# Kernel optimization log

Measured on AMD Instinct MI355X. Metric: run time of the kernel, lower is better.

The kernel has to match this reference:

```python
import jax, jax.numpy as jnp
import numpy as np

N_NODES = 10000
N_EDGES = 160000
NEG_SLOPE = 0.2  # PyG GATConv default leaky_relu slope


def gat_conv(x, src, dst, W, a_src, a_dst, b, heads, out_ch, concat, n):
    # linear projection per head: [n, heads, out_ch]
    h = (x @ W).reshape(n, heads, out_ch)
    # per-node attention logits
    al_s = jnp.sum(h * a_src, axis=-1)  # [n, heads]
    al_d = jnp.sum(h * a_dst, axis=-1)  # [n, heads]
    # per-edge score, softmax over incoming edges of each destination node
    e = jax.nn.leaky_relu(al_s[src] + al_d[dst], NEG_SLOPE)  # [E, heads]
    m = jax.ops.segment_max(e, dst, num_segments=n)
    p = jnp.exp(e - m[dst])
    s = jax.ops.segment_sum(p, dst, num_segments=n)
    alpha = p / (s[dst] + 1e-16)  # [E, heads]
    # weighted scatter-aggregate of source messages
    out = jax.ops.segment_sum(h[src] * alpha[..., None], dst, num_segments=n)
    out = out.reshape(n, heads * out_ch) if concat else out.mean(axis=1)
    return out + b


def setup_inputs() -> dict:
    key = jax.random.key(0)
    ks = jax.random.split(key, 16)
    x = jax.random.normal(ks[0], (N_NODES, 32), dtype=jnp.float32)
    edge_index = jax.random.randint(ks[1], (2, N_EDGES), 0, N_NODES, dtype=jnp.int64)

    def glorot(k, shape):
        fan = shape[0] + shape[-1]
        return jax.random.uniform(k, shape, jnp.float32, -1.0, 1.0) * jnp.sqrt(6.0 / fan)

    # layer 1: 32 -> 8 per head, 8 heads, concat -> 64
    W1 = glorot(ks[2], (32, 64))
    asrc1 = glorot(ks[3], (8, 8))
    adst1 = glorot(ks[4], (8, 8))
    b1 = jnp.zeros((64,), jnp.float32)
    # layer 2: 64 -> 64 per head, 8 heads, concat -> 512
    W2 = glorot(ks[5], (64, 512))
    asrc2 = glorot(ks[6], (8, 64))
    adst2 = glorot(ks[7], (8, 64))
    b2 = jnp.zeros((512,), jnp.float32)
    # layer 3: 512 -> 6, 1 head, no concat
    W3 = glorot(ks[8], (512, 6))
    asrc3 = glorot(ks[9], (1, 6))
    adst3 = glorot(ks[10], (1, 6))
    b3 = jnp.zeros((6,), jnp.float32)

    return dict(x=x, edge_index=edge_index,
                W1=W1, asrc1=asrc1, adst1=adst1, b1=b1,
                W2=W2, asrc2=asrc2, adst2=adst2, b2=b2,
                W3=W3, asrc3=asrc3, adst3=adst3, b3=b3)


def reference(x, edge_index, W1, asrc1, adst1, b1, W2, asrc2, adst2, b2, W3, asrc3, adst3, b3):
    n = x.shape[0]
    # PyG GATConv adds self-loops by default
    loops = jnp.arange(n, dtype=edge_index.dtype)
    src = jnp.concatenate([edge_index[0], loops])
    dst = jnp.concatenate([edge_index[1], loops])
    # dropout layers are identity in eval mode
    h = jax.nn.elu(gat_conv(x, src, dst, W1, asrc1, adst1, b1, 8, 8, True, n))
    h = jax.nn.elu(gat_conv(h, src, dst, W2, asrc2, adst2, b2, 8, 64, True, n))
    out = gat_conv(h, src, dst, W3, asrc3, adst3, b3, 1, 6, False, n)
    return out
```

## Files before the change

kernel.cpp:

```cpp
#include <hip/hip_runtime.h>
#include <hip/hip_bf16.h>
#include <math.h>


#define NEG_SLOPE 0.2f

__device__ __forceinline__ float lrelu(float v) {
  return v > 0.f ? v : NEG_SLOPE * v;
}


__global__ __launch_bounds__(256) void count_deg(const int* __restrict__ ei,
                                                 int* __restrict__ deg, int E) {
  int e = blockIdx.x * blockDim.x + threadIdx.x;
  if (e < E) atomicAdd(&deg[ei[E + e]], 1);
}

__global__ __launch_bounds__(1024) void scan3(const int* __restrict__ deg,
                                              int* __restrict__ rowptr,
                                              int* __restrict__ cursor, int n,
                                              const float* __restrict__ W1,
                                              const float* __restrict__ as1,
                                              const float* __restrict__ ad1,
                                              const float* __restrict__ W2,
                                              const float* __restrict__ as2,
                                              const float* __restrict__ ad2,
                                              float* __restrict__ av) {
  int t = threadIdx.x;
  if (blockIdx.x == 0) {
    __shared__ int part[1024];
    int chunk = (n + 1023) >> 10;
    int lo = t * chunk;
    int hi = min(lo + chunk, n);
    int s = 0;
    for (int i = lo; i < hi; ++i) s += deg[i];
    part[t] = s;
    __syncthreads();
    for (int off = 1; off < 1024; off <<= 1) {
      int v = (t >= off) ? part[t - off] : 0;
      __syncthreads();
      part[t] += v;
      __syncthreads();
    }
    int run = (t == 0) ? 0 : part[t - 1];
    for (int i = lo; i < hi; ++i) {
      rowptr[i] = run;
      cursor[i] = run;
      run += deg[i];
    }
    if (t == 1023) rowptr[n] = part[1023];
  } else if (blockIdx.x == 1) {
    if (t < 256) {
      int h = t >> 5, k = t & 31;
      float s = 0.f, d = 0.f;
#pragma unroll
      for (int c = 0; c < 8; ++c) {
        float w = W1[k * 64 + h * 8 + c];
        s += w * as1[h * 8 + c];
        d += w * ad1[h * 8 + c];
      }
      av[t] = s;
      av[256 + t] = d;
    }
  } else {
    if (t < 512) {
      int h = t >> 6, k = t & 63;
      float s = 0.f, d = 0.f;
#pragma unroll
      for (int c = 0; c < 64; ++c) {
        float w = W2[k * 512 + h * 64 + c];
        s += w * as2[h * 64 + c];
        d += w * ad2[h * 64 + c];
      }
      av[512 + t] = s;
      av[1024 + t] = d;
    }
  }
}

__global__ __launch_bounds__(256) void fill_edges(const int* __restrict__ ei,
                                                  int* __restrict__ cursor,
                                                  int* __restrict__ esrc, int E) {
  int e = blockIdx.x * blockDim.x + threadIdx.x;
  if (e < E) {
    int d = ei[E + e];
    int pos = atomicAdd(&cursor[d], 1);
    esrc[pos] = ei[e];
  }
}


template <int HH, int K>
__global__ __launch_bounds__(256) void logits_x(const float* __restrict__ X,
                                                const float* __restrict__ avs,
                                                const float* __restrict__ avd,
                                                float* __restrict__ als,
                                                float* __restrict__ ald,
                                                float* __restrict__ selfe, int n) {
  int idx = blockIdx.x * blockDim.x + threadIdx.x;
  if (idx >= n * HH) return;
  int node = idx / HH;
  int h = idx - node * HH;
  const float* xr = X + (size_t)node * K;
  const float* vs = avs + h * K;
  const float* vd = avd + h * K;
  float s0 = 0.f, s1 = 0.f;
#pragma unroll
  for (int k4 = 0; k4 < K / 4; ++k4) {
    float4 xv = *reinterpret_cast<const float4*>(&xr[k4 * 4]);
    float4 a = *reinterpret_cast<const float4*>(&vs[k4 * 4]);
    float4 b = *reinterpret_cast<const float4*>(&vd[k4 * 4]);
    s0 += xv.x * a.x + xv.y * a.y + xv.z * a.z + xv.w * a.w;
    s1 += xv.x * b.x + xv.y * b.y + xv.z * b.z + xv.w * b.w;
  }
  als[idx] = s0;
  ald[idx] = s1;
  float e = s0 + s1;
  selfe[idx] = lrelu(e);
}


__global__ __launch_bounds__(256) void msum_alpha8(const int* __restrict__ esrc,
                                                   const float* __restrict__ als,
                                                   const float* __restrict__ ald,
                                                   const float* __restrict__ selfe,
                                                   const int* __restrict__ rowptr,
                                                   float* __restrict__ alpha,
                                                   float* __restrict__ asel, int n) {
  int node = blockIdx.x * 4 + (threadIdx.x >> 6);
  int lane = threadIdx.x & 63;
  if (node >= n) return;
  int i = lane >> 3;
  int h = lane & 7;
  float aldv = ald[node * 8 + h];
  float e0 = selfe[node * 8 + h];
  int r0 = rowptr[node], r1 = rowptr[node + 1];

  float m = e0;
  for (int p = r0 + i; p < r1; p += 8)
    m = fmaxf(m, lrelu(als[esrc[p] * 8 + h] + aldv));
  m = fmaxf(m, __shfl_xor(m, 8, 64));
  m = fmaxf(m, __shfl_xor(m, 16, 64));
  m = fmaxf(m, __shfl_xor(m, 32, 64));

  float s = 0.f;
  for (int p = r0 + i; p < r1; p += 8)
    s += __expf(lrelu(als[esrc[p] * 8 + h] + aldv) - m);
  s += __shfl_xor(s, 8, 64);
  s += __shfl_xor(s, 16, 64);
  s += __shfl_xor(s, 32, 64);
  float a0 = __expf(e0 - m);
  float rs = 1.f / (s + a0 + 1e-16f);
  if (lane < 8) asel[node * 8 + lane] = a0 * rs;

  for (int p = r0 + i; p < r1; p += 8)
    alpha[(size_t)p * 8 + h] = __expf(lrelu(als[esrc[p] * 8 + h] + aldv) - m) * rs;
}

__global__ __launch_bounds__(256) void msum_alpha1(const int* __restrict__ esrc,
                                                   const float* __restrict__ als,
                                                   const float* __restrict__ ald,
                                                   const float* __restrict__ selfe,
                                                   const int* __restrict__ rowptr,
                                                   float* __restrict__ alpha,
                                                   float* __restrict__ asel, int n) {
  int node = blockIdx.x * 4 + (threadIdx.x >> 6);
  int lane = threadIdx.x & 63;
  if (node >= n) return;
  float aldv = ald[node];
  float e0 = selfe[node];
  int r0 = rowptr[node], r1 = rowptr[node + 1];

  float m = e0;
  for (int p = r0 + lane; p < r1; p += 64)
    m = fmaxf(m, lrelu(als[esrc[p]] + aldv));
#pragma unroll
  for (int off = 1; off < 64; off <<= 1) m = fmaxf(m, __shfl_xor(m, off, 64));

  float s = 0.f;
  for (int p = r0 + lane; p < r1; p += 64)
    s += __expf(lrelu(als[esrc[p]] + aldv) - m);
#pragma unroll
  for (int off = 1; off < 64; off <<= 1) s += __shfl_xor(s, off, 64);
  float a0 = __expf(e0 - m);
  float rs = 1.f / (s + a0 + 1e-16f);
  if (lane == 0) asel[node] = a0 * rs;

  for (int p = r0 + lane; p < r1; p += 64)
    alpha[p] = __expf(lrelu(als[esrc[p]] + aldv) - m) * rs;
}


__global__ __launch_bounds__(256) void agg1(const float* __restrict__ X,
                                            const float* __restrict__ alpha,
                                            const float* __restrict__ asel,
                                            const int* __restrict__ rowptr,
                                            const int* __restrict__ esrc,
                                            float* __restrict__ AGG, int n) {
  int node = blockIdx.x * 4 + (threadIdx.x >> 6);
  int lane = threadIdx.x & 63;
  if (node >= n) return;
  int ch = lane & 31;
  int eslot = lane >> 5;
  float acc[8];
  if (eslot == 0) {
    float xs = X[((unsigned)node << 5) + ch];
#pragma unroll
    for (int h = 0; h < 8; ++h) acc[h] = asel[node * 8 + h] * xs;
  } else {
#pragma unroll
    for (int h = 0; h < 8; ++h) acc[h] = 0.f;
  }
  int r0 = rowptr[node], r1 = rowptr[node + 1];
  int p = r0 + eslot;
  for (; p + 2 < r1; p += 4) {
    int s0 = esrc[p], s1 = esrc[p + 2];
    float xv0 = X[((unsigned)s0 << 5) + ch];
    float xv1 = X[((unsigned)s1 << 5) + ch];
    float4 a00 = *reinterpret_cast<const float4*>(&alpha[(size_t)p * 8]);
    float4 a01 = *reinterpret_cast<const float4*>(&alpha[(size_t)p * 8 + 4]);
    float4 a10 = *reinterpret_cast<const float4*>(&alpha[(size_t)(p + 2) * 8]);
    float4 a11 = *reinterpret_cast<const float4*>(&alpha[(size_t)(p + 2) * 8 + 4]);
    acc[0] += a00.x * xv0; acc[1] += a00.y * xv0;
    acc[2] += a00.z * xv0; acc[3] += a00.w * xv0;
    acc[4] += a01.x * xv0; acc[5] += a01.y * xv0;
    acc[6] += a01.z * xv0; acc[7] += a01.w * xv0;
    acc[0] += a10.x * xv1; acc[1] += a10.y * xv1;
    acc[2] += a10.z * xv1; acc[3] += a10.w * xv1;
    acc[4] += a11.x * xv1; acc[5] += a11.y * xv1;
    acc[6] += a11.z * xv1; acc[7] += a11.w * xv1;
  }
  if (p < r1) {
    int s0 = esrc[p];
    float xv0 = X[((unsigned)s0 << 5) + ch];
    float4 a00 = *reinterpret_cast<const float4*>(&alpha[(size_t)p * 8]);
    float4 a01 = *reinterpret_cast<const float4*>(&alpha[(size_t)p * 8 + 4]);
    acc[0] += a00.x * xv0; acc[1] += a00.y * xv0;
    acc[2] += a00.z * xv0; acc[3] += a00.w * xv0;
    acc[4] += a01.x * xv0; acc[5] += a01.y * xv0;
    acc[6] += a01.z * xv0; acc[7] += a01.w * xv0;
  }
#pragma unroll
  for (int h = 0; h < 8; ++h) acc[h] += __shfl_xor(acc[h], 32, 64);
  if (eslot == 0) {
    unsigned base = (unsigned)node * 256 + ch;
#pragma unroll
    for (int h = 0; h < 8; ++h) AGG[base + h * 32] = acc[h];
  }
}

__global__ __launch_bounds__(256) void agg2(const float* __restrict__ X,
                                            const float* __restrict__ alpha,
                                            const float* __restrict__ asel,
                                            const int* __restrict__ rowptr,
                                            const int* __restrict__ esrc,
                                            float* __restrict__ AGG, int n) {
  int node = blockIdx.x * 4 + (threadIdx.x >> 6);
  int lane = threadIdx.x & 63;
  if (node >= n) return;
  float acc[8];
  float xs = X[((unsigned)node << 6) + lane];
#pragma unroll
  for (int h = 0; h < 8; ++h) acc[h] = asel[node * 8 + h] * xs;
  int r0 = rowptr[node], r1 = rowptr[node + 1];
  int p = r0;
  for (; p + 4 <= r1; p += 4) {
    int s0 = esrc[p], s1 = esrc[p + 1], s2 = esrc[p + 2], s3 = esrc[p + 3];
    float xv0 = X[((unsigned)s0 << 6) + lane];
    float xv1 = X[((unsigned)s1 << 6) + lane];
    float xv2 = X[((unsigned)s2 << 6) + lane];
    float xv3 = X[((unsigned)s3 << 6) + lane];
#pragma unroll
    for (int q = 0; q < 4; ++q) {
      float xv = q == 0 ? xv0 : q == 1 ? xv1 : q == 2 ? xv2 : xv3;
      float4 a0 = *reinterpret_cast<const float4*>(&alpha[(size_t)(p + q) * 8]);
      float4 a1 = *reinterpret_cast<const float4*>(&alpha[(size_t)(p + q) * 8 + 4]);
      acc[0] += a0.x * xv; acc[1] += a0.y * xv;
      acc[2] += a0.z * xv; acc[3] += a0.w * xv;
      acc[4] += a1.x * xv; acc[5] += a1.y * xv;
      acc[6] += a1.z * xv; acc[7] += a1.w * xv;
    }
  }
  for (; p < r1; ++p) {
    int s0 = esrc[p];
    float xv = X[((unsigned)s0 << 6) + lane];
    float4 a0 = *reinterpret_cast<const float4*>(&alpha[(size_t)p * 8]);
    float4 a1 = *reinterpret_cast<const float4*>(&alpha[(size_t)p * 8 + 4]);
    acc[0] += a0.x * xv; acc[1] += a0.y * xv;
    acc[2] += a0.z * xv; acc[3] += a0.w * xv;
    acc[4] += a1.x * xv; acc[5] += a1.y * xv;
    acc[6] += a1.z * xv; acc[7] += a1.w * xv;
  }
  unsigned base = (unsigned)node * 512 + lane;
#pragma unroll
  for (int h = 0; h < 8; ++h) AGG[base + h * 64] = acc[h];
}


__global__ __launch_bounds__(256) void proj1(const float* __restrict__ AGG,
                                             const float* __restrict__ W1,
                                             const float* __restrict__ b1,
                                             float* __restrict__ OUT, int n) {
  int w = blockIdx.x * 4 + (threadIdx.x >> 6);
  int lane = threadIdx.x & 63;
  int node0 = w * 8;
  if (node0 >= n) return;
  int h = lane >> 3;
  float acc[8];
#pragma unroll
  for (int j = 0; j < 8; ++j) acc[j] = 0.f;
  for (int k = 0; k < 32; ++k) {
    float wv = W1[k * 64 + lane];
#pragma unroll
    for (int j = 0; j < 8; ++j) {
      int nd = min(node0 + j, n - 1);
      acc[j] += AGG[(unsigned)nd * 256 + h * 32 + k] * wv;
    }
  }
  float bv = b1[lane];
#pragma unroll
  for (int j = 0; j < 8; ++j) {
    int nd = node0 + j;
    if (nd >= n) break;
    float v = acc[j] + bv;
    v = v > 0.f ? v : expm1f(v);
    OUT[(unsigned)nd * 64 + lane] = v;
  }
}

__global__ __launch_bounds__(256) void proj2(const float* __restrict__ AGG,
                                             const float* __restrict__ W2,
                                             const float* __restrict__ b2,
                                             float* __restrict__ OUT, int n) {
  int w = blockIdx.x * 4 + (threadIdx.x >> 6);
  int lane = threadIdx.x & 63;
  int node0 = w * 4;
  if (node0 >= n) return;
  int c0 = lane * 8;
  int h = lane >> 3;
  float acc[4][8];
#pragma unroll
  for (int j = 0; j < 4; ++j)
#pragma unroll
    for (int c = 0; c < 8; ++c) acc[j][c] = 0.f;
  for (int k = 0; k < 64; ++k) {
    const float4 w0 = *reinterpret_cast<const float4*>(&W2[(size_t)k * 512 + c0]);
    const float4 w1 = *reinterpret_cast<const float4*>(&W2[(size_t)k * 512 + c0 + 4]);
#pragma unroll
    for (int j = 0; j < 4; ++j) {
      int nd = min(node0 + j, n - 1);
      float xv = AGG[(unsigned)nd * 512 + h * 64 + k];
      acc[j][0] += xv * w0.x; acc[j][1] += xv * w0.y;
      acc[j][2] += xv * w0.z; acc[j][3] += xv * w0.w;
      acc[j][4] += xv * w1.x; acc[j][5] += xv * w1.y;
      acc[j][6] += xv * w1.z; acc[j][7] += xv * w1.w;
    }
  }
  float4 bv0 = *reinterpret_cast<const float4*>(&b2[c0]);
  float4 bv1 = *reinterpret_cast<const float4*>(&b2[c0 + 4]);
#pragma unroll
  for (int j = 0; j < 4; ++j) {
    int nd = node0 + j;
    if (nd >= n) break;
    float v[8];
    v[0] = acc[j][0] + bv0.x; v[1] = acc[j][1] + bv0.y;
    v[2] = acc[j][2] + bv0.z; v[3] = acc[j][3] + bv0.w;
    v[4] = acc[j][4] + bv1.x; v[5] = acc[j][5] + bv1.y;
    v[6] = acc[j][6] + bv1.z; v[7] = acc[j][7] + bv1.w;
#pragma unroll
    for (int c = 0; c < 8; ++c) v[c] = v[c] > 0.f ? v[c] : expm1f(v[c]);
    float4* o = reinterpret_cast<float4*>(&OUT[(unsigned)nd * 512 + c0]);
    o[0] = make_float4(v[0], v[1], v[2], v[3]);
    o[1] = make_float4(v[4], v[5], v[6], v[7]);
  }
}

__global__ __launch_bounds__(256) void gemm_l3f(const float* __restrict__ X,
                                                const float* __restrict__ W,
                                                const float* __restrict__ As,
                                                const float* __restrict__ Ad,
                                                float* __restrict__ H,
                                                float* __restrict__ als,
                                                float* __restrict__ ald,
                                                float* __restrict__ selfe, int n) {
  int node = blockIdx.x * 4 + (threadIdx.x >> 6);
  int lane = threadIdx.x & 63;
  if (node >= n) return;
  float acc[6] = {0.f, 0.f, 0.f, 0.f, 0.f, 0.f};
  for (int k = lane; k < 512; k += 64) {
    float xv = X[(size_t)node * 512 + k];
#pragma unroll
    for (int c = 0; c < 6; ++c) acc[c] += xv * W[k * 6 + c];
  }
#pragma unroll
  for (int c = 0; c < 6; ++c) {
#pragma unroll
    for (int off = 32; off >= 1; off >>= 1)
      acc[c] += __shfl_down(acc[c], off, 64);
  }
  if (lane == 0) {
    float s0 = 0.f, s1 = 0.f;
#pragma unroll
    for (int c = 0; c < 6; ++c) {
      H[(size_t)node * 6 + c] = acc[c];
      s0 += acc[c] * As[c];
      s1 += acc[c] * Ad[c];
    }
    als[node] = s0;
    ald[node] = s1;
    selfe[node] = lrelu(s0 + s1);
  }
}

__global__ __launch_bounds__(256) void agg_l3(const float* __restrict__ HF,
                                              const float* __restrict__ alpha,
                                              const float* __restrict__ asel,
                                              const float* __restrict__ bias,
                                              const int* __restrict__ rowptr,
                                              const int* __restrict__ esrc,
                                              float* __restrict__ OUT, int n) {
  int node = blockIdx.x * 4 + (threadIdx.x >> 6);
  int lane = threadIdx.x & 63;
  if (node >= n) return;
  int ch = lane < 6 ? lane : 0;
  float acc = asel[node] * HF[(unsigned)node * 6u + ch];
  int r0 = rowptr[node], r1 = rowptr[node + 1];
  int p = r0;
  for (; p + 2 <= r1; p += 2) {
    int s0 = esrc[p], s1 = esrc[p + 1];
    float h0 = HF[(unsigned)s0 * 6u + ch];
    float h1 = HF[(unsigned)s1 * 6u + ch];
    acc += alpha[p] * h0 + alpha[p + 1] * h1;
  }
  if (p < r1) acc += alpha[p] * HF[(unsigned)esrc[p] * 6u + ch];
  if (lane < 6) OUT[(unsigned)node * 6u + lane] = acc + bias[lane];
}


extern "C" void kernel_launch(void* const* d_in, const int* in_sizes, int n_in,
                              void* d_out, int out_size, void* d_ws, size_t ws_size,
                              hipStream_t stream) {
  const float* x     = (const float*)d_in[0];
  const int*   ei    = (const int*)d_in[1];
  const float* W1    = (const float*)d_in[2];
  const float* asrc1 = (const float*)d_in[3];
  const float* adst1 = (const float*)d_in[4];
  const float* b1    = (const float*)d_in[5];
  const float* W2    = (const float*)d_in[6];
  const float* asrc2 = (const float*)d_in[7];
  const float* adst2 = (const float*)d_in[8];
  const float* b2    = (const float*)d_in[9];
  const float* W3    = (const float*)d_in[10];
  const float* asrc3 = (const float*)d_in[11];
  const float* adst3 = (const float*)d_in[12];
  const float* b3    = (const float*)d_in[13];
  float* outf = (float*)d_out;

  const int n = in_sizes[0] / 32;
  const int E = in_sizes[1] / 2;

  char* ws = (char*)d_ws;
  size_t off = 0;
  auto alloc = [&](size_t bytes) {
    size_t o = off;
    off = (off + bytes + 255) & ~(size_t)255;
    return ws + o;
  };
  int* deg     = (int*)alloc((size_t)n * 4);
  int* rowptr  = (int*)alloc((size_t)(n + 1) * 4);
  int* cursor  = (int*)alloc((size_t)n * 4);
  int* esrc    = (int*)alloc((size_t)E * 4);
  float* alpha = (float*)alloc((size_t)E * 8 * 4);
  float* selfe = (float*)alloc((size_t)n * 8 * 4);
  float* als   = (float*)alloc((size_t)n * 8 * 4);
  float* ald   = (float*)alloc((size_t)n * 8 * 4);
  float* asel  = (float*)alloc((size_t)n * 8 * 4);
  float* av    = (float*)alloc((size_t)1536 * 4);
  float* AGG1  = (float*)alloc((size_t)n * 256 * 4);
  float* x1    = (float*)alloc((size_t)n * 64 * 4);
  float* AGG2  = (float*)alloc((size_t)n * 512 * 4);
  float* x2    = (float*)alloc((size_t)n * 512 * 4);
  float* h3    = (float*)alloc((size_t)n * 6 * 4);

  int nb4 = (n + 3) / 4;

  hipMemsetAsync(deg, 0, (size_t)n * 4, stream);
  count_deg<<<(E + 255) / 256, 256, 0, stream>>>(ei, deg, E);
  scan3<<<3, 1024, 0, stream>>>(deg, rowptr, cursor, n,
                                W1, asrc1, adst1, W2, asrc2, adst2, av);
  fill_edges<<<(E + 255) / 256, 256, 0, stream>>>(ei, cursor, esrc, E);

  logits_x<8, 32><<<(n * 8 + 255) / 256, 256, 0, stream>>>(x, av, av + 256, als, ald, selfe, n);
  msum_alpha8<<<nb4, 256, 0, stream>>>(esrc, als, ald, selfe, rowptr, alpha, asel, n);
  agg1<<<nb4, 256, 0, stream>>>(x, alpha, asel, rowptr, esrc, AGG1, n);
  proj1<<<(n / 8 + 3) / 4 + 1, 256, 0, stream>>>(AGG1, W1, b1, x1, n);

  logits_x<8, 64><<<(n * 8 + 255) / 256, 256, 0, stream>>>(x1, av + 512, av + 1024, als, ald, selfe, n);
  msum_alpha8<<<nb4, 256, 0, stream>>>(esrc, als, ald, selfe, rowptr, alpha, asel, n);
  agg2<<<nb4, 256, 0, stream>>>(x1, alpha, asel, rowptr, esrc, AGG2, n);
  proj2<<<(n / 4 + 3) / 4 + 1, 256, 0, stream>>>(AGG2, W2, b2, x2, n);

  gemm_l3f<<<nb4, 256, 0, stream>>>(x2, W3, asrc3, adst3, h3, als, ald, selfe, n);
  msum_alpha1<<<nb4, 256, 0, stream>>>(esrc, als, ald, selfe, rowptr, alpha, asel, n);
  agg_l3<<<nb4, 256, 0, stream>>>(h3, alpha, asel, b3, rowptr, esrc, outf, n);
}
```

Measured before the change: 256.4 us.

## Fuse whole GAT pipeline into one cooperative persistent kernel with grid syncs

Replaces the chain of about fifteen kernel launches with a single cooperative kernel that uses grid.sync between phases. Within each layer it fuses the softmax, the aggregation and the projection, keeping per-node attention weights and aggregates in shared memory so the alpha and AGG intermediates no longer pass through global memory. The goal is to remove launch overhead and that global traffic. In exchange, occupancy is bounded by the cooperative grid size, each grid-wide barrier has a cost, and nodes with more than 96 incoming edges fall back to recomputing exponentials for the overflow edges.

New measurement: 782.0 us. 3.05x slower.

```diff
diff --git a/kernel.cpp b/kernel.cpp
--- a/kernel.cpp
+++ b/kernel.cpp
@@ -1,12 +1,401 @@
 #include <hip/hip_runtime.h>
 #include <hip/hip_bf16.h>
+#include <hip/hip_cooperative_groups.h>
 #include <math.h>
 
 
 #define NEG_SLOPE 0.2f
+#define DCAP 96
+
+namespace cg = cooperative_groups;
 
 __device__ __forceinline__ float lrelu(float v) {
   return v > 0.f ? v : NEG_SLOPE * v;
+}
+
+
+struct CoopP {
+  const float* x; const int* ei;
+  const float* W1; const float* as1; const float* ad1; const float* b1;
+  const float* W2; const float* as2; const float* ad2; const float* b2;
+  const float* W3; const float* as3; const float* ad3; const float* b3;
+  float* outf;
+  int n, E;
+  int* deg; int* rowptr; int* cursor; int* esrc;
+  float* als; float* ald; float* selfe; float* av;
+  float* x1; float* x2; float* h3;
+};
+
+template <int K>
+__device__ __forceinline__ void logits_one(const float* __restrict__ X,
+                                           const float* __restrict__ avs,
+                                           const float* __restrict__ avd,
+                                           float* __restrict__ als,
+                                           float* __restrict__ ald,
+                                           float* __restrict__ selfe, int idx) {
+  int node = idx >> 3;
+  int h = idx & 7;
+  const float* xr = X + (size_t)node * K;
+  const float* vs = avs + h * K;
+  const float* vd = avd + h * K;
+  float s0 = 0.f, s1 = 0.f;
+#pragma unroll
+  for (int k4 = 0; k4 < K / 4; ++k4) {
+    float4 xv = *reinterpret_cast<const float4*>(&xr[k4 * 4]);
+    float4 a = *reinterpret_cast<const float4*>(&vs[k4 * 4]);
+    float4 b = *reinterpret_cast<const float4*>(&vd[k4 * 4]);
+    s0 += xv.x * a.x + xv.y * a.y + xv.z * a.z + xv.w * a.w;
+    s1 += xv.x * b.x + xv.y * b.y + xv.z * b.z + xv.w * b.w;
+  }
+  als[idx] = s0;
+  ald[idx] = s1;
+  selfe[idx] = lrelu(s0 + s1);
+}
+
+__global__ __launch_bounds__(256, 4) void gat_coop(CoopP P) {
+  cg::grid_group grid = cg::this_grid();
+  const int t = threadIdx.x;
+  const int lane = t & 63;
+  const int w = t >> 6;
+  const int bid = blockIdx.x;
+  const int nb = gridDim.x;
+  const int tid = bid * 256 + t;
+  const int nthr = nb * 256;
+  const int wid = bid * 4 + w;
+  const int nwv = nb * 4;
+  const int n = P.n, E = P.E;
+
+  __shared__ __align__(16) float s_alpha[4][DCAP * 8];
+  __shared__ __align__(16) float s_AGG[8][512];
+  __shared__ float s_sel[4][8], s_m[4][8], s_rs[4][8];
+  __shared__ int s_scan[256];
+
+  for (int i = tid; i < n; i += nthr) P.deg[i] = 0;
+  grid.sync();
+
+  for (int e = tid; e < E; e += nthr) atomicAdd(&P.deg[P.ei[E + e]], 1);
+  grid.sync();
+
+  if (bid == 0) {
+    int chunk = (n + 255) >> 8;
+    int lo = t * chunk;
+    int hi = min(lo + chunk, n);
+    int s = 0;
+    for (int i = lo; i < hi; ++i) s += P.deg[i];
+    s_scan[t] = s;
+    __syncthreads();
+    for (int off = 1; off < 256; off <<= 1) {
+      int v = (t >= off) ? s_scan[t - off] : 0;
+      __syncthreads();
+      s_scan[t] += v;
+      __syncthreads();
+    }
+    int run = (t == 0) ? 0 : s_scan[t - 1];
+    for (int i = lo; i < hi; ++i) {
+      P.rowptr[i] = run;
+      P.cursor[i] = run;
+      run += P.deg[i];
+    }
+    if (t == 255) P.rowptr[n] = s_scan[255];
+  } else if (bid == 1) {
+    int h = t >> 5, k = t & 31;
+    float s = 0.f, d = 0.f;
+#pragma unroll
+    for (int c = 0; c < 8; ++c) {
+      float wv = P.W1[k * 64 + h * 8 + c];
+      s += wv * P.as1[h * 8 + c];
+      d += wv * P.ad1[h * 8 + c];
+    }
+    P.av[t] = s;
+    P.av[256 + t] = d;
+  } else if (bid == 2) {
+    for (int idx = t; idx < 512; idx += 256) {
+      int h = idx >> 6, k = idx & 63;
+      float s = 0.f, d = 0.f;
+#pragma unroll
+      for (int c = 0; c < 64; ++c) {
+        float wv = P.W2[(size_t)k * 512 + h * 64 + c];
+        s += wv * P.as2[h * 64 + c];
+        d += wv * P.ad2[h * 64 + c];
+      }
+      P.av[512 + idx] = s;
+      P.av[1024 + idx] = d;
+    }
+  }
+  grid.sync();
+
+  for (int e = tid; e < E; e += nthr) {
+    int d = P.ei[E + e];
+    int pos = atomicAdd(&P.cursor[d], 1);
+    P.esrc[pos] = P.ei[e];
+  }
+  for (int idx = tid; idx < n * 8; idx += nthr)
+    logits_one<32>(P.x, P.av, P.av + 256, P.als, P.ald, P.selfe, idx);
+  grid.sync();
+
+  for (int nd = wid; nd < n; nd += nwv) {
+    int r0 = P.rowptr[nd], r1 = P.rowptr[nd + 1];
+    int i = lane >> 3, h = lane & 7;
+    float aldv = P.ald[nd * 8 + h];
+    float e0 = P.selfe[nd * 8 + h];
+    float m = e0;
+    for (int p = r0 + i; p < r1; p += 8)
+      m = fmaxf(m, lrelu(P.als[P.esrc[p] * 8 + h] + aldv));
+    m = fmaxf(m, __shfl_xor(m, 8, 64));
+    m = fmaxf(m, __shfl_xor(m, 16, 64));
+    m = fmaxf(m, __shfl_xor(m, 32, 64));
+    float s = 0.f;
+    for (int p = r0 + i; p < r1; p += 8)
+      s += __expf(lrelu(P.als[P.esrc[p] * 8 + h] + aldv) - m);
+    s += __shfl_xor(s, 8, 64);
+    s += __shfl_xor(s, 16, 64);
+    s += __shfl_xor(s, 32, 64);
+    float a0 = __expf(e0 - m);
+    float rs = 1.f / (s + a0 + 1e-16f);
+    if (i == 0) {
+      s_sel[w][h] = a0 * rs;
+      s_m[w][h] = m;
+      s_rs[w][h] = rs;
+    }
+    for (int p = r0 + i; p < r1; p += 8) {
+      int o = p - r0;
+      if (o < DCAP)
+        s_alpha[w][o * 8 + h] = __expf(lrelu(P.als[P.esrc[p] * 8 + h] + aldv) - m) * rs;
+    }
+    int ch = lane & 31, es = lane >> 5;
+    float acc[8];
+    {
+      float xs = (es == 0) ? P.x[(size_t)nd * 32 + ch] : 0.f;
+#pragma unroll
+      for (int q = 0; q < 8; ++q) acc[q] = s_sel[w][q] * xs;
+    }
+    for (int p = r0 + es; p < r1; p += 2) {
+      int src = P.esrc[p];
+      float xv = P.x[(size_t)src * 32 + ch];
+      int o = p - r0;
+      if (o < DCAP) {
+        const float4* ap = reinterpret_cast<const float4*>(&s_alpha[w][o * 8]);
+        float4 av0 = ap[0], av1 = ap[1];
+        acc[0] += av0.x * xv; acc[1] += av0.y * xv;
+        acc[2] += av0.z * xv; acc[3] += av0.w * xv;
+        acc[4] += av1.x * xv; acc[5] += av1.y * xv;
+        acc[6] += av1.z * xv; acc[7] += av1.w * xv;
+      } else {
+#pragma unroll
+        for (int q = 0; q < 8; ++q) {
+          float ev = lrelu(P.als[src * 8 + q] + P.ald[nd * 8 + q]);
+          acc[q] += __expf(ev - s_m[w][q]) * s_rs[w][q] * xv;
+        }
+      }
+    }
+#pragma unroll
+    for (int q = 0; q < 8; ++q) acc[q] += __shfl_xor(acc[q], 32, 64);
+    if (es == 0) {
+#pragma unroll
+      for (int q = 0; q < 8; ++q) s_AGG[w][q * 32 + ch] = acc[q];
+    }
+    int col = lane, hc = col >> 3;
+    float pa = 0.f;
+    for (int k = 0; k < 32; ++k)
+      pa += s_AGG[w][hc * 32 + k] * P.W1[k * 64 + col];
+    float v = pa + P.b1[col];
+    v = v > 0.f ? v : expm1f(v);
+    P.x1[(size_t)nd * 64 + col] = v;
+  }
+  grid.sync();
+
+  for (int idx = tid; idx < n * 8; idx += nthr)
+    logits_one<64>(P.x1, P.av + 512, P.av + 1024, P.als, P.ald, P.selfe, idx);
+  grid.sync();
+
+  int ngrp = (n + 7) >> 3;
+  for (int g = bid; g < ngrp; g += nb) {
+    for (int j = 0; j < 2; ++j) {
+      int nd = g * 8 + w * 2 + j;
+      if (nd < n) {
+        int r0 = P.rowptr[nd], r1 = P.rowptr[nd + 1];
+        int i = lane >> 3, h = lane & 7;
+        float aldv = P.ald[nd * 8 + h];
+        float e0 = P.selfe[nd * 8 + h];
+        float m = e0;
+        for (int p = r0 + i; p < r1; p += 8)
+          m = fmaxf(m, lrelu(P.als[P.esrc[p] * 8 + h] + aldv));
+        m = fmaxf(m, __shfl_xor(m, 8, 64));
+        m = fmaxf(m, __shfl_xor(m, 16, 64));
+        m = fmaxf(m, __shfl_xor(m, 32, 64));
+        float s = 0.f;
+        for (int p = r0 + i; p < r1; p += 8)
+          s += __expf(lrelu(P.als[P.esrc[p] * 8 + h] + aldv) - m);
+        s += __shfl_xor(s, 8, 64);
+        s += __shfl_xor(s, 16, 64);
+        s += __shfl_xor(s, 32, 64);
+        float a0 = __expf(e0 - m);
+        float rs = 1.f / (s + a0 + 1e-16f);
+        if (i == 0) {
+          s_sel[w][h] = a0 * rs;
+          s_m[w][h] = m;
+          s_rs[w][h] = rs;
+        }
+        for (int p = r0 + i; p < r1; p += 8) {
+          int o = p - r0;
+          if (o < DCAP)
+            s_alpha[w][o * 8 + h] = __expf(lrelu(P.als[P.esrc[p] * 8 + h] + aldv) - m) * rs;
+        }
+        float acc[8];
+        float xs = P.x1[(size_t)nd * 64 + lane];
+#pragma unroll
+        for (int q = 0; q < 8; ++q) acc[q] = s_sel[w][q] * xs;
+        int p = r0;
+        for (; p + 2 <= r1; p += 2) {
+          int s0i = P.esrc[p], s1i = P.esrc[p + 1];
+          float xv0 = P.x1[(size_t)s0i * 64 + lane];
+          float xv1 = P.x1[(size_t)s1i * 64 + lane];
+          int o0 = p - r0, o1 = o0 + 1;
+          if (o1 < DCAP) {
+            const float4* a0p = reinterpret_cast<const float4*>(&s_alpha[w][o0 * 8]);
+            const float4* a1p = reinterpret_cast<const float4*>(&s_alpha[w][o1 * 8]);
+            float4 a00 = a0p[0], a01 = a0p[1], a10 = a1p[0], a11 = a1p[1];
+            acc[0] += a00.x * xv0; acc[1] += a00.y * xv0;
+            acc[2] += a00.z * xv0; acc[3] += a00.w * xv0;
+            acc[4] += a01.x * xv0; acc[5] += a01.y * xv0;
+            acc[6] += a01.z * xv0; acc[7] += a01.w * xv0;
+            acc[0] += a10.x * xv1; acc[1] += a10.y * xv1;
+            acc[2] += a10.z * xv1; acc[3] += a10.w * xv1;
+            acc[4] += a11.x * xv1; acc[5] += a11.y * xv1;
+            acc[6] += a11.z * xv1; acc[7] += a11.w * xv1;
+          } else {
+#pragma unroll
+            for (int q = 0; q < 8; ++q) {
+              float ev0 = lrelu(P.als[s0i * 8 + q] + P.ald[nd * 8 + q]);
+              float ev1 = lrelu(P.als[s1i * 8 + q] + P.ald[nd * 8 + q]);
+              acc[q] += __expf(ev0 - s_m[w][q]) * s_rs[w][q] * xv0;
+              acc[q] += __expf(ev1 - s_m[w][q]) * s_rs[w][q] * xv1;
+            }
+          }
+        }
+        if (p < r1) {
+          int s0i = P.esrc[p];
+          float xv0 = P.x1[(size_t)s0i * 64 + lane];
+          int o0 = p - r0;
+          if (o0 < DCAP) {
+            const float4* a0p = reinterpret_cast<const float4*>(&s_alpha[w][o0 * 8]);
+            float4 a00 = a0p[0], a01 = a0p[1];
+            acc[0] += a00.x * xv0; acc[1] += a00.y * xv0;
+            acc[2] += a00.z * xv0; acc[3] += a00.w * xv0;
+            acc[4] += a01.x * xv0; acc[5] += a01.y * xv0;
+            acc[6] += a01.z * xv0; acc[7] += a01.w * xv0;
+          } else {
+#pragma unroll
+            for (int q = 0; q < 8; ++q) {
+              float ev0 = lrelu(P.als[s0i * 8 + q] + P.ald[nd * 8 + q]);
+              acc[q] += __expf(ev0 - s_m[w][q]) * s_rs[w][q] * xv0;
+            }
+          }
+        }
+#pragma unroll
+        for (int q = 0; q < 8; ++q) s_AGG[w * 2 + j][q * 64 + lane] = acc[q];
+      }
+    }
+    __syncthreads();
+    {
+      int cg_ = lane, jg = w;
+      int c0 = cg_ * 8, hc = cg_ >> 3;
+      int n0 = g * 8 + jg * 2;
+      float pa[2][8];
+#pragma unroll
+      for (int jj = 0; jj < 2; ++jj)
+#pragma unroll
+        for (int c = 0; c < 8; ++c) pa[jj][c] = 0.f;
+      for (int k = 0; k < 64; ++k) {
+        float4 w0 = *reinterpret_cast<const float4*>(&P.W2[(size_t)k * 512 + c0]);
+        float4 w1 = *reinterpret_cast<const float4*>(&P.W2[(size_t)k * 512 + c0 + 4]);
+        float xa = s_AGG[jg * 2][hc * 64 + k];
+        float xb = s_AGG[jg * 2 + 1][hc * 64 + k];
+        pa[0][0] += xa * w0.x; pa[0][1] += xa * w0.y;
+        pa[0][2] += xa * w0.z; pa[0][3] += xa * w0.w;
+        pa[0][4] += xa * w1.x; pa[0][5] += xa * w1.y;
+        pa[0][6] += xa * w1.z; pa[0][7] += xa * w1.w;
+        pa[1][0] += xb * w0.x; pa[1][1] += xb * w0.y;
+        pa[1][2] += xb * w0.z; pa[1][3] += xb * w0.w;
+        pa[1][4] += xb * w1.x; pa[1][5] += xb * w1.y;
+        pa[1][6] += xb * w1.z; pa[1][7] += xb * w1.w;
+      }
+      float4 bv0 = *reinterpret_cast<const float4*>(&P.b2[c0]);
+      float4 bv1 = *reinterpret_cast<const float4*>(&P.b2[c0 + 4]);
+#pragma unroll
+      for (int jj = 0; jj < 2; ++jj) {
+        int nd = n0 + jj;
+        if (nd < n) {
+          float vv[8];
+          vv[0] = pa[jj][0] + bv0.x; vv[1] = pa[jj][1] + bv0.y;
+          vv[2] = pa[jj][2] + bv0.z; vv[3] = pa[jj][3] + bv0.w;
+          vv[4] = pa[jj][4] + bv1.x; vv[5] = pa[jj][5] + bv1.y;
+          vv[6] = pa[jj][6] + bv1.z; vv[7] = pa[jj][7] + bv1.w;
+#pragma unroll
+          for (int c = 0; c < 8; ++c) vv[c] = vv[c] > 0.f ? vv[c] : expm1f(vv[c]);
+          float4* o = reinterpret_cast<float4*>(&P.x2[(size_t)nd * 512 + c0]);
+          o[0] = make_float4(vv[0], vv[1], vv[2], vv[3]);
+          o[1] = make_float4(vv[4], vv[5], vv[6], vv[7]);
+        }
+      }
+    }
+    __syncthreads();
+  }
+  grid.sync();
+
+  for (int nd = wid; nd < n; nd += nwv) {
+    float a6[6] = {0.f, 0.f, 0.f, 0.f, 0.f, 0.f};
+    for (int k = lane; k < 512; k += 64) {
+      float xv = P.x2[(size_t)nd * 512 + k];
+#pragma unroll
+      for (int c = 0; c < 6; ++c) a6[c] += xv * P.W3[k * 6 + c];
+    }
+#pragma unroll
+    for (int c = 0; c < 6; ++c) {
+#pragma unroll
+      for (int off = 32; off >= 1; off >>= 1)
+        a6[c] += __shfl_down(a6[c], off, 64);
+    }
+    if (lane == 0) {
+      float s0 = 0.f, s1 = 0.f;
+#pragma unroll
+      for (int c = 0; c < 6; ++c) {
+        P.h3[(size_t)nd * 6 + c] = a6[c];
+        s0 += a6[c] * P.as3[c];
+        s1 += a6[c] * P.ad3[c];
+      }
+      P.als[nd] = s0;
+      P.ald[nd] = s1;
+      P.selfe[nd] = lrelu(s0 + s1);
+    }
+  }
+  grid.sync();
+
+  for (int nd = wid; nd < n; nd += nwv) {
+    int r0 = P.rowptr[nd], r1 = P.rowptr[nd + 1];
+    float aldv = P.ald[nd];
+    float e0 = P.selfe[nd];
+    float m = e0;
+    for (int p = r0 + lane; p < r1; p += 64)
+      m = fmaxf(m, lrelu(P.als[P.esrc[p]] + aldv));
+#pragma unroll
+    for (int off = 1; off < 64; off <<= 1) m = fmaxf(m, __shfl_xor(m, off, 64));
+    float s = 0.f;
+    for (int p = r0 + lane; p < r1; p += 64)
+      s += __expf(lrelu(P.als[P.esrc[p]] + aldv) - m);
+#pragma unroll
+    for (int off = 1; off < 64; off <<= 1) s += __shfl_xor(s, off, 64);
+    float a0 = __expf(e0 - m);
+    float rs = 1.f / (s + a0 + 1e-16f);
+    int ch = lane < 6 ? lane : 0;
+    float acc = a0 * rs * P.h3[(size_t)nd * 6 + ch];
+    for (int p = r0; p < r1; ++p) {
+      int src = P.esrc[p];
+      float ev = lrelu(P.als[src] + aldv);
+      acc += __expf(ev - m) * rs * P.h3[(size_t)src * 6 + ch];
+    }
+    if (lane < 6) P.outf[(size_t)nd * 6 + lane] = acc + P.b3[lane];
+  }
 }
 
 
@@ -55,9 +444,9 @@
       float s = 0.f, d = 0.f;
 #pragma unroll
       for (int c = 0; c < 8; ++c) {
-        float w = W1[k * 64 + h * 8 + c];
-        s += w * as1[h * 8 + c];
-        d += w * ad1[h * 8 + c];
+        float wv = W1[k * 64 + h * 8 + c];
+        s += wv * as1[h * 8 + c];
+        d += wv * ad1[h * 8 + c];
       }
       av[t] = s;
       av[256 + t] = d;
@@ -68,9 +457,9 @@
       float s = 0.f, d = 0.f;
 #pragma unroll
       for (int c = 0; c < 64; ++c) {
-        float w = W2[k * 512 + h * 64 + c];
-        s += w * as2[h * 64 + c];
-        d += w * ad2[h * 64 + c];
+        float wv = W2[(size_t)k * 512 + h * 64 + c];
+        s += wv * as2[h * 64 + c];
+        d += wv * ad2[h * 64 + c];
       }
       av[512 + t] = s;
       av[1024 + t] = d;
@@ -88,7 +477,6 @@
     esrc[pos] = ei[e];
   }
 }
-
 
 template <int HH, int K>
 __global__ __launch_bounds__(256) void logits_x(const float* __restrict__ X,
@@ -115,10 +503,8 @@
   }
   als[idx] = s0;
   ald[idx] = s1;
-  float e = s0 + s1;
-  selfe[idx] = lrelu(e);
-}
-
+  selfe[idx] = lrelu(s0 + s1);
+}
 
 __global__ __launch_bounds__(256) void msum_alpha8(const int* __restrict__ esrc,
                                                    const float* __restrict__ als,
@@ -135,14 +521,12 @@
   float aldv = ald[node * 8 + h];
   float e0 = selfe[node * 8 + h];
   int r0 = rowptr[node], r1 = rowptr[node + 1];
-
   float m = e0;
   for (int p = r0 + i; p < r1; p += 8)
     m = fmaxf(m, lrelu(als[esrc[p] * 8 + h] + aldv));
   m = fmaxf(m, __shfl_xor(m, 8, 64));
   m = fmaxf(m, __shfl_xor(m, 16, 64));
   m = fmaxf(m, __shfl_xor(m, 32, 64));
-
   float s = 0.f;
   for (int p = r0 + i; p < r1; p += 8)
     s += __expf(lrelu(als[esrc[p] * 8 + h] + aldv) - m);
@@ -152,7 +536,6 @@
   float a0 = __expf(e0 - m);
   float rs = 1.f / (s + a0 + 1e-16f);
   if (lane < 8) asel[node * 8 + lane] = a0 * rs;
-
   for (int p = r0 + i; p < r1; p += 8)
     alpha[(size_t)p * 8 + h] = __expf(lrelu(als[esrc[p] * 8 + h] + aldv) - m) * rs;
 }
@@ -170,13 +553,11 @@
   float aldv = ald[node];
   float e0 = selfe[node];
   int r0 = rowptr[node], r1 = rowptr[node + 1];
-
   float m = e0;
   for (int p = r0 + lane; p < r1; p += 64)
     m = fmaxf(m, lrelu(als[esrc[p]] + aldv));
 #pragma unroll
   for (int off = 1; off < 64; off <<= 1) m = fmaxf(m, __shfl_xor(m, off, 64));
-
   float s = 0.f;
   for (int p = r0 + lane; p < r1; p += 64)
     s += __expf(lrelu(als[esrc[p]] + aldv) - m);
@@ -185,11 +566,9 @@
   float a0 = __expf(e0 - m);
   float rs = 1.f / (s + a0 + 1e-16f);
   if (lane == 0) asel[node] = a0 * rs;
-
   for (int p = r0 + lane; p < r1; p += 64)
     alpha[p] = __expf(lrelu(als[esrc[p]] + aldv) - m) * rs;
 }
-
 
 __global__ __launch_bounds__(256) void agg1(const float* __restrict__ X,
                                             const float* __restrict__ alpha,
@@ -295,7 +674,6 @@
 #pragma unroll
   for (int h = 0; h < 8; ++h) AGG[base + h * 64] = acc[h];
 }
-
 
 __global__ __launch_bounds__(256) void proj1(const float* __restrict__ AGG,
                                              const float* __restrict__ W1,
@@ -482,25 +860,60 @@
   float* x2    = (float*)alloc((size_t)n * 512 * 4);
   float* h3    = (float*)alloc((size_t)n * 6 * 4);
 
-  int nb4 = (n + 3) / 4;
-
-  hipMemsetAsync(deg, 0, (size_t)n * 4, stream);
-  count_deg<<<(E + 255) / 256, 256, 0, stream>>>(ei, deg, E);
-  scan3<<<3, 1024, 0, stream>>>(deg, rowptr, cursor, n,
-                                W1, asrc1, adst1, W2, asrc2, adst2, av);
-  fill_edges<<<(E + 255) / 256, 256, 0, stream>>>(ei, cursor, esrc, E);
-
-  logits_x<8, 32><<<(n * 8 + 255) / 256, 256, 0, stream>>>(x, av, av + 256, als, ald, selfe, n);
-  msum_alpha8<<<nb4, 256, 0, stream>>>(esrc, als, ald, selfe, rowptr, alpha, asel, n);
-  agg1<<<nb4, 256, 0, stream>>>(x, alpha, asel, rowptr, esrc, AGG1, n);
-  proj1<<<(n / 8 + 3) / 4 + 1, 256, 0, stream>>>(AGG1, W1, b1, x1, n);
-
-  logits_x<8, 64><<<(n * 8 + 255) / 256, 256, 0, stream>>>(x1, av + 512, av + 1024, als, ald, selfe, n);
-  msum_alpha8<<<nb4, 256, 0, stream>>>(esrc, als, ald, selfe, rowptr, alpha, asel, n);
-  agg2<<<nb4, 256, 0, stream>>>(x1, alpha, asel, rowptr, esrc, AGG2, n);
-  proj2<<<(n / 4 + 3) / 4 + 1, 256, 0, stream>>>(AGG2, W2, b2, x2, n);
-
-  gemm_l3f<<<nb4, 256, 0, stream>>>(x2, W3, asrc3, adst3, h3, als, ald, selfe, n);
-  msum_alpha1<<<nb4, 256, 0, stream>>>(esrc, als, ald, selfe, rowptr, alpha, asel, n);
-  agg_l3<<<nb4, 256, 0, stream>>>(h3, alpha, asel, b3, rowptr, esrc, outf, n);
-}
+  bool coop_done = false;
+  {
+    int dev = 0;
+    (void)hipGetDevice(&dev);
+    int cus = 0;
+    (void)hipDeviceGetAttribute(&cus, hipDeviceAttributeMultiprocessorCount, dev);
+    int nbpc = 0;
+    hipError_t oe = hipOccupancyMaxActiveBlocksPerMultiprocessor(
+        &nbpc, reinterpret_cast<const void*>(gat_coop), 256, 0);
+    if (oe == hipSuccess && nbpc > 0 && cus > 0) {
+      int gridsz = nbpc * cus;
+      if (gridsz > 2048) gridsz = 2048;
+      if (gridsz >= 8) {
+        CoopP P;
+        P.x = x; P.ei = ei;
+        P.W1 = W1; P.as1 = asrc1; P.ad1 = adst1; P.b1 = b1;
+        P.W2 = W2; P.as2 = asrc2; P.ad2 = adst2; P.b2 = b2;
+        P.W3 = W3; P.as3 = asrc3; P.ad3 = adst3; P.b3 = b3;
+        P.outf = outf; P.n = n; P.E = E;
+        P.deg = deg; P.rowptr = rowptr; P.cursor = cursor; P.esrc = esrc;
+        P.als = als; P.ald = ald; P.selfe = selfe; P.av = av;
+        P.x1 = x1; P.x2 = x2; P.h3 = h3;
+        void* args[] = { &P };
+        hipError_t rc = hipLaunchCooperativeKernel(
+            reinterpret_cast<const void*>(gat_coop), dim3(gridsz), dim3(256),
+            args, 0, stream);
+        if (rc == hipSuccess) coop_done = true;
+        else (void)hipGetLastError();
+      }
+    } else {
+      (void)hipGetLastError();
+    }
+  }
+
+  if (!coop_done) {
+    int nb4 = (n + 3) / 4;
+    hipMemsetAsync(deg, 0, (size_t)n * 4, stream);
+    count_deg<<<(E + 255) / 256, 256, 0, stream>>>(ei, deg, E);
+    scan3<<<3, 1024, 0, stream>>>(deg, rowptr, cursor, n,
+                                  W1, asrc1, adst1, W2, asrc2, adst2, av);
+    fill_edges<<<(E + 255) / 256, 256, 0, stream>>>(ei, cursor, esrc, E);
+
+    logits_x<8, 32><<<(n * 8 + 255) / 256, 256, 0, stream>>>(x, av, av + 256, als, ald, selfe, n);
+    msum_alpha8<<<nb4, 256, 0, stream>>>(esrc, als, ald, selfe, rowptr, alpha, asel, n);
+    agg1<<<nb4, 256, 0, stream>>>(x, alpha, asel, rowptr, esrc, AGG1, n);
+    proj1<<<(n / 8 + 3) / 4 + 1, 256, 0, stream>>>(AGG1, W1, b1, x1, n);
+
+    logits_x<8, 64><<<(n * 8 + 255) / 256, 256, 0, stream>>>(x1, av + 512, av + 1024, als, ald, selfe, n);
+    msum_alpha8<<<nb4, 256, 0, stream>>>(esrc, als, ald, selfe, rowptr, alpha, asel, n);
+    agg2<<<nb4, 256, 0, stream>>>(x1, alpha, asel, rowptr, esrc, AGG2, n);
+    proj2<<<(n / 4 + 3) / 4 + 1, 256, 0, stream>>>(AGG2, W2, b2, x2, n);
+
+    gemm_l3f<<<nb4, 256, 0, stream>>>(x2, W3, asrc3, adst3, h3, als, ald, selfe, n);
+    msum_alpha1<<<nb4, 256, 0, stream>>>(esrc, als, ald, selfe, rowptr, alpha, asel, n);
+    agg_l3<<<nb4, 256, 0, stream>>>(h3, alpha, asel, b3, rowptr, esrc, outf, n);
+  }
+}
```
